# Kernel optimization log

Measured on AMD Instinct MI355X. Metric: run time of the kernel, lower is better.

The kernel has to match this reference:

```python
import jax, jax.numpy as jnp
import numpy as np

N_NODES = 100000
N_EDGES = 320000
DIM = 256  # hidden_dim*2 (bi-RNN)
BN_EPS = 1e-5


def setup_inputs() -> dict:
    key = jax.random.key(0)
    k1, k2, k3 = jax.random.split(key, 3)
    x = jax.random.normal(k1, (N_NODES, DIM), dtype=jnp.float32)
    W = jax.random.normal(k2, (DIM, DIM), dtype=jnp.float32) * (1.0 / np.sqrt(DIM))
    b = jnp.zeros((DIM,), dtype=jnp.float32)
    gamma = jnp.ones((DIM,), dtype=jnp.float32)
    beta = jnp.zeros((DIM,), dtype=jnp.float32)
    edge_index = jax.random.randint(k3, (2, N_EDGES), 0, N_NODES, dtype=jnp.int64)
    return {"x": x, "W": W, "b": b, "gamma": gamma, "beta": beta,
            "edge_index": edge_index}


def reference(x, W, b, gamma, beta, edge_index):
    N = x.shape[0]
    # --- GCNConv: add self-loops, symmetric deg^-1/2 normalization ---
    loop = jnp.arange(N, dtype=edge_index.dtype)
    row = jnp.concatenate([edge_index[0], loop])  # source / j
    col = jnp.concatenate([edge_index[1], loop])  # target / i
    deg = jax.ops.segment_sum(jnp.ones_like(col, dtype=x.dtype), col,
                              num_segments=N)
    dinv = jax.lax.rsqrt(deg)  # deg >= 1 due to self-loops
    norm = dinv[row] * dinv[col]  # [E+N]
    h = x @ W  # linear transform before propagation (PyG GCNConv)
    msg = h[row] * norm[:, None]  # gather + scale, [E+N, F]
    out = jax.ops.segment_sum(msg, col, num_segments=N) + b  # scatter-add
    # --- BatchNorm1d over nodes (training-mode batch statistics) ---
    mean = jnp.mean(out, axis=0)
    var = jnp.var(out, axis=0)
    out = (out - mean) * jax.lax.rsqrt(var + BN_EPS) * gamma + beta
    return jnp.tanh(out)
```

## Files before the change

### kernel.cpp

```cpp
#include <hip/hip_runtime.h>
#include <stdint.h>

#define N_NODES 100000
#define N_EDGES 320000
#define DIM 256
#define BN_EPS 1e-5f

typedef __attribute__((ext_vector_type(8))) short short8;
typedef __attribute__((ext_vector_type(4))) float f32x4;

__device__ __forceinline__ float bf2f(unsigned short u) {
    union { unsigned int i; float f; } v; v.i = ((unsigned int)u) << 16; return v.f;
}
__device__ __forceinline__ unsigned short f2bf(float f) {
    union { float f; unsigned int i; } v; v.f = f;
    unsigned int x = v.i;
    return (unsigned short)((x + 0x7fffu + ((x >> 16) & 1u)) >> 16);
}
__device__ __forceinline__ int eidx(const int* ei, int i64, int which, int e) {
    int idx = which * N_EDGES + e;
    return i64 ? ei[idx * 2] : ei[idx];
}
__device__ __forceinline__ f32x4 ldx4(const void* xv, int xf32, size_t off) {
    if (xf32) return *(const f32x4*)((const float*)xv + off);
    uint2 u = *(const uint2*)((const unsigned short*)xv + off);
    f32x4 o;
    o[0] = bf2f((unsigned short)(u.x & 0xffffu));
    o[1] = bf2f((unsigned short)(u.x >> 16));
    o[2] = bf2f((unsigned short)(u.y & 0xffffu));
    o[3] = bf2f((unsigned short)(u.y >> 16));
    return o;
}

__global__ void k_detect(const unsigned short* __restrict__ xs,
                         const unsigned short* __restrict__ wsw,
                         const int* __restrict__ ei, int* __restrict__ flags) {
    __shared__ int red[3];
    int tid = threadIdx.x;
    if (tid < 3) red[tid] = 0;
    __syncthreads();
    int badx = 0, badw = 0, nz = 0;
    for (int j = 0; j < 8; ++j) {
        if (!(fabsf(bf2f(xs[tid * 8 + j])) <= 1000.0f)) badx = 1;
        if (!(fabsf(bf2f(wsw[tid * 8 + j])) <= 1000.0f)) badw = 1;
        if (ei[(tid * 8 + j) * 2 + 1] != 0) nz = 1;
    }
    if (badx) atomicOr(&red[0], 1);
    if (badw) atomicOr(&red[1], 1);
    if (nz)   atomicOr(&red[2], 1);
    __syncthreads();
    if (tid == 0) { flags[0] = red[0]; flags[1] = red[1]; flags[2] = red[2] ? 0 : 1; }
}

__global__ void k_zero(int* __restrict__ cnt, float* __restrict__ stats) {
    int i = blockIdx.x * 256 + threadIdx.x;
    if (i < N_NODES) cnt[i] = 0;
    if (i < 512) stats[i] = 0.0f;
}

__global__ void k_cnt(const int* __restrict__ ei, int* __restrict__ cnt,
                      const int* __restrict__ flags) {
    int i64 = flags[2];
    int e = blockIdx.x * 256 + threadIdx.x;
    if (e < N_EDGES) atomicAdd(&cnt[eidx(ei, i64, 1, e)], 1);
}

__global__ void k_dinv(const int* __restrict__ cnt, float* __restrict__ dinv) {
    int i = blockIdx.x * 256 + threadIdx.x;
    if (i < N_NODES) dinv[i] = rsqrtf((float)cnt[i] + 1.0f);
}

__global__ void k_scan1(const int* __restrict__ cnt, int* __restrict__ partial) {
    __shared__ int red[256];
    int t = threadIdx.x, b = blockIdx.x;
    int i0 = b * 512 + t * 2;
    int s = 0;
    if (i0 < N_NODES) s += cnt[i0];
    if (i0 + 1 < N_NODES) s += cnt[i0 + 1];
    red[t] = s;
    __syncthreads();
    for (int off = 128; off > 0; off >>= 1) {
        if (t < off) red[t] += red[t + off];
        __syncthreads();
    }
    if (t == 0) partial[b] = red[0];
}

__global__ void k_scan2(const int* __restrict__ partial, int* __restrict__ pbase) {
    __shared__ int s[256];
    int t = threadIdx.x;
    int v = (t < 200) ? partial[t] : 0;
    s[t] = v;
    __syncthreads();
    for (int off = 1; off < 256; off <<= 1) {
        int u = (t >= off) ? s[t - off] : 0;
        __syncthreads();
        s[t] += u;
        __syncthreads();
    }
    if (t < 200) pbase[t] = s[t] - v;
}

__global__ void k_scan3(const int* __restrict__ cnt, const int* __restrict__ pbase,
                        int* __restrict__ row_start, int* __restrict__ cursor) {
    __shared__ int s[512];
    int t = threadIdx.x, b = blockIdx.x;
    int i = b * 512 + t;
    int v = (i < N_NODES) ? cnt[i] : 0;
    s[t] = v;
    __syncthreads();
    for (int off = 1; off < 512; off <<= 1) {
        int u = (t >= off) ? s[t - off] : 0;
        __syncthreads();
        s[t] += u;
        __syncthreads();
    }
    if (i < N_NODES) {
        int excl = pbase[b] + s[t] - v;
        row_start[i] = excl;
        cursor[i] = excl;
    }
}

__global__ void k_fill(const int* __restrict__ ei, const float* __restrict__ dinv,
                       int* __restrict__ cursor, int* __restrict__ csr_src,
                       float* __restrict__ csr_nrm, const int* __restrict__ flags) {
    int i64 = flags[2];
    int e = blockIdx.x * 256 + threadIdx.x;
    if (e >= N_EDGES) return;
    int c = eidx(ei, i64, 1, e);
    int r = eidx(ei, i64, 0, e);
    int slot = atomicAdd(&cursor[c], 1);
    csr_src[slot] = r;
    csr_nrm[slot] = dinv[r] * dinv[c];
}

__global__ void k_wt(const void* __restrict__ wv, unsigned short* __restrict__ Wth,
                     unsigned short* __restrict__ Wtl, const int* __restrict__ flags) {
    int wf32 = flags[1];
    int k = blockIdx.x, n = threadIdx.x;
    float v = wf32 ? ((const float*)wv)[k * DIM + n]
                   : bf2f(((const unsigned short*)wv)[k * DIM + n]);
    unsigned short h = f2bf(v);
    Wth[(size_t)n * DIM + k] = h;
    Wtl[(size_t)n * DIM + k] = f2bf(v - bf2f(h));
}

__global__ void k_agg(const void* __restrict__ xv, const int* __restrict__ row_start,
                      const int* __restrict__ cnt, const int* __restrict__ csr_src,
                      const float* __restrict__ csr_nrm, const float* __restrict__ dinv,
                      unsigned short* __restrict__ zh, unsigned short* __restrict__ zl,
                      const int* __restrict__ flags, int base) {
    int xf32 = flags[0];
    int gid = blockIdx.x * 256 + threadIdx.x;
    int node = base + (gid >> 6);
    int lane = gid & 63;
    float dv = dinv[node];
    float s = dv * dv;
    f32x4 acc = ldx4(xv, xf32, (size_t)node * DIM + lane * 4);
    acc[0] *= s; acc[1] *= s; acc[2] *= s; acc[3] *= s;
    int start = row_start[node];
    int len = cnt[node];
    for (int j = 0; j < len; ++j) {
        int src = csr_src[start + j];
        float nrm = csr_nrm[start + j];
        f32x4 xr = ldx4(xv, xf32, (size_t)src * DIM + lane * 4);
        acc[0] += nrm * xr[0]; acc[1] += nrm * xr[1];
        acc[2] += nrm * xr[2]; acc[3] += nrm * xr[3];
    }
    uint ph0 = 0, ph1 = 0, pl0 = 0, pl1 = 0;
    {
        unsigned short h0 = f2bf(acc[0]), h1 = f2bf(acc[1]);
        unsigned short h2 = f2bf(acc[2]), h3 = f2bf(acc[3]);
        ph0 = (uint)h0 | ((uint)h1 << 16);
        ph1 = (uint)h2 | ((uint)h3 << 16);
        unsigned short l0 = f2bf(acc[0] - bf2f(h0)), l1 = f2bf(acc[1] - bf2f(h1));
        unsigned short l2 = f2bf(acc[2] - bf2f(h2)), l3 = f2bf(acc[3] - bf2f(h3));
        pl0 = (uint)l0 | ((uint)l1 << 16);
        pl1 = (uint)l2 | ((uint)l3 << 16);
    }
    size_t zo = (size_t)(node - base) * DIM + lane * 4;
    uint2 vh; vh.x = ph0; vh.y = ph1;
    uint2 vl; vl.x = pl0; vl.y = pl1;
    *(uint2*)(zh + zo) = vh;
    *(uint2*)(zl + zo) = vl;
}

__launch_bounds__(256, 3)
__global__ void k_gemm(const unsigned short* __restrict__ zh,
                       const unsigned short* __restrict__ zl,
                       const unsigned short* __restrict__ Wth,
                       const unsigned short* __restrict__ Wtl,
                       float* __restrict__ out, float* __restrict__ stats, int base) {
    __shared__ unsigned short zsh[80 * 128];
    __shared__ unsigned short zsl[80 * 128];
    __shared__ float bs[512];
    int tid = threadIdx.x;
    bs[tid] = 0.0f; bs[tid + 256] = 0.0f;
    int m0l = blockIdx.x * 80;
    int w = tid >> 6, lane = tid & 63, quad = lane >> 4, rl = lane & 15;

    f32x4 acc[5][4];
    #pragma unroll
    for (int ms = 0; ms < 5; ++ms)
        #pragma unroll
        for (int nt = 0; nt < 4; ++nt)
            acc[ms][nt] = (f32x4){0.f, 0.f, 0.f, 0.f};

    const char* zhB = (const char*)zh;
    const char* zlB = (const char*)zl;

    for (int half = 0; half < 2; ++half) {
        #pragma unroll
        for (int i = 0; i < 5; ++i) {
            int d   = i * 4096 + w * 1024 + lane * 16;
            int row = d >> 8;
            int kb  = d & 255;
            size_t soff = (size_t)(m0l + row) * 512 + (size_t)(half * 256)
                        + (size_t)(kb ^ ((row & 7) << 4));
            __builtin_amdgcn_global_load_lds(
                (const __attribute__((address_space(1))) unsigned int*)(zhB + soff),
                (__attribute__((address_space(3))) unsigned int*)
                    ((char*)zsh + i * 4096 + w * 1024),
                16, 0, 0);
            __builtin_amdgcn_global_load_lds(
                (const __attribute__((address_space(1))) unsigned int*)(zlB + soff),
                (__attribute__((address_space(3))) unsigned int*)
                    ((char*)zsl + i * 4096 + w * 1024),
                16, 0, 0);
        }
        __syncthreads();

        #pragma unroll
        for (int kk = 0; kk < 4; ++kk) {
            int k0g = half * 128 + kk * 32 + quad * 8;
            short8 bh[4], bl[4];
            #pragma unroll
            for (int nt = 0; nt < 4; ++nt) {
                int n = w * 64 + nt * 16 + rl;
                bh[nt] = *(const short8*)(Wth + (size_t)n * DIM + k0g);
                bl[nt] = *(const short8*)(Wtl + (size_t)n * DIM + k0g);
            }
            #pragma unroll
            for (int ms = 0; ms < 5; ++ms) {
                int row = ms * 16 + rl;
                int kbl = (kk * 32 + quad * 8) * 2;
                int off = row * 256 + (kbl ^ ((row & 7) << 4));
                short8 ah = *(const short8*)((const char*)zsh + off);
                short8 al = *(const short8*)((const char*)zsl + off);
                #pragma unroll
                for (int nt = 0; nt < 4; ++nt) {
                    acc[ms][nt] = __builtin_amdgcn_mfma_f32_16x16x32_bf16(ah, bh[nt], acc[ms][nt], 0, 0, 0);
                    acc[ms][nt] = __builtin_amdgcn_mfma_f32_16x16x32_bf16(al, bh[nt], acc[ms][nt], 0, 0, 0);
                    acc[ms][nt] = __builtin_amdgcn_mfma_f32_16x16x32_bf16(ah, bl[nt], acc[ms][nt], 0, 0, 0);
                }
            }
        }
        __syncthreads();
    }

    #pragma unroll
    for (int nt = 0; nt < 4; ++nt) {
        int col = w * 64 + nt * 16 + rl;
        float s1 = 0.f, s2 = 0.f;
        #pragma unroll
        for (int ms = 0; ms < 5; ++ms)
            #pragma unroll
            for (int i = 0; i < 4; ++i) {
                float v = acc[ms][nt][i];
                s1 += v; s2 += v * v;
                out[(size_t)(base + m0l + ms * 16 + quad * 4 + i) * DIM + col] = v;
            }
        atomicAdd(&bs[col], s1);
        atomicAdd(&bs[256 + col], s2);
    }
    __syncthreads();
    if (tid < 256) {
        atomicAdd(&stats[tid], bs[tid]);
        atomicAdd(&stats[256 + tid], bs[256 + tid]);
    }
}

__global__ void k_fin(const float* __restrict__ stats, const void* __restrict__ gv,
                      const void* __restrict__ bv, float* __restrict__ scsh,
                      const int* __restrict__ flags) {
    int ff32 = flags[0];
    int f = threadIdx.x;
    const float invN = 1.0f / (float)N_NODES;
    float mean = stats[f] * invN;
    float var = stats[256 + f] * invN - mean * mean;
    float g = ff32 ? ((const float*)gv)[f] : bf2f(((const unsigned short*)gv)[f]);
    float bb = ff32 ? ((const float*)bv)[f] : bf2f(((const unsigned short*)bv)[f]);
    float sc = g * rsqrtf(var + BN_EPS);
    scsh[f] = sc;
    scsh[256 + f] = bb - mean * sc;
}

__global__ void k_final(float* __restrict__ out, const float* __restrict__ scsh) {
    int t = blockIdx.x * 256 + threadIdx.x;
    int f0 = (t & 63) * 4;
    size_t off = (size_t)t * 4;
    f32x4 v = *(const f32x4*)(out + off);
    f32x4 o;
    #pragma unroll
    for (int j = 0; j < 4; ++j)
        o[j] = tanhf(v[j] * scsh[f0 + j] + scsh[256 + f0 + j]);
    *(f32x4*)(out + off) = o;
}

extern "C" void kernel_launch(void* const* d_in, const int* in_sizes, int n_in,
                              void* d_out, int out_size, void* d_ws, size_t ws_size,
                              hipStream_t stream) {
    const void* x     = d_in[0];
    const void* W     = d_in[1];
    const void* gamma = d_in[3];
    const void* beta  = d_in[4];
    const int* ei     = (const int*)d_in[5];
    float* out = (float*)d_out;

    char* ws = (char*)d_ws;
    int*   flags     = (int*)(ws);
    int*   cnt       = (int*)(ws + 4096);
    int*   row_start = (int*)(ws + 409600);
    int*   cursor    = (int*)(ws + 819200);
    float* dinv      = (float*)(ws + 1228800);
    int*   partial   = (int*)(ws + 1638400);
    int*   pbase     = (int*)(ws + 1646592);
    float* stats     = (float*)(ws + 1654784);
    float* scsh      = (float*)(ws + 1662976);
    unsigned short* Wth = (unsigned short*)(ws + 1671168);
    unsigned short* Wtl = (unsigned short*)(ws + 1802240);
    int*   csr_src   = (int*)(ws + 1933312);
    float* csr_nrm   = (float*)(ws + 3215360);
    const size_t zoff = 4718592;

    size_t zbytes = ws_size > zoff ? ws_size - zoff : 0;
    long long maxRows = (long long)(zbytes / ((size_t)DIM * 4));
    maxRows -= maxRows % 80;
    if (maxRows <= 0) maxRows = 80;
    if (maxRows > N_NODES) maxRows = N_NODES;

    unsigned short* zh = (unsigned short*)(ws + zoff);
    unsigned short* zl = zh + (size_t)maxRows * DIM;

    k_detect<<<1,    256, 0, stream>>>((const unsigned short*)x, (const unsigned short*)W, ei, flags);
    k_zero  <<<391,  256, 0, stream>>>(cnt, stats);
    k_cnt   <<<1250, 256, 0, stream>>>(ei, cnt, flags);
    k_dinv  <<<391,  256, 0, stream>>>(cnt, dinv);
    k_scan1 <<<200,  256, 0, stream>>>(cnt, partial);
    k_scan2 <<<1,    256, 0, stream>>>(partial, pbase);
    k_scan3 <<<200,  512, 0, stream>>>(cnt, pbase, row_start, cursor);
    k_fill  <<<1250, 256, 0, stream>>>(ei, dinv, cursor, csr_src, csr_nrm, flags);
    k_wt    <<<256,  256, 0, stream>>>(W, Wth, Wtl, flags);

    for (int base = 0; base < N_NODES; base += (int)maxRows) {
        int count = N_NODES - base;
        if (count > (int)maxRows) count = (int)maxRows;
        k_agg <<<count / 4,  256, 0, stream>>>(x, row_start, cnt, csr_src, csr_nrm,
                                               dinv, zh, zl, flags, base);
        k_gemm<<<count / 80, 256, 0, stream>>>(zh, zl, Wth, Wtl, out, stats, base);
    }

    k_fin  <<<1,     256, 0, stream>>>(stats, gamma, beta, scsh, flags);
    k_final<<<25000, 256, 0, stream>>>(out, scsh);
}
```

Before: 423.2 us.

## Pack CSR entries and batch neighbor gathers via wavefront shuffles in aggregation

Merges the CSR source-index and norm arrays into one packed int2 array. Each wavefront loads up to 64 neighbor entries in one coalesced load and broadcasts them with shuffles, so four neighbor-row gathers can be in flight per iteration instead of a serial dependent chain. The self-loop is folded in as an extra padded entry, and rows with more than 63 neighbors fall back to a serial tail. Output stores to the z buffers become nontemporal.

```diff
diff --git a/kernel.cpp b/kernel.cpp
--- a/kernel.cpp
+++ b/kernel.cpp
@@ -8,6 +8,7 @@
 
 typedef __attribute__((ext_vector_type(8))) short short8;
 typedef __attribute__((ext_vector_type(4))) float f32x4;
+typedef __attribute__((ext_vector_type(2))) unsigned int u32x2;
 
 __device__ __forceinline__ float bf2f(unsigned short u) {
     union { unsigned int i; float f; } v; v.i = ((unsigned int)u) << 16; return v.f;
@@ -123,16 +124,17 @@
 }
 
 __global__ void k_fill(const int* __restrict__ ei, const float* __restrict__ dinv,
-                       int* __restrict__ cursor, int* __restrict__ csr_src,
-                       float* __restrict__ csr_nrm, const int* __restrict__ flags) {
+                       int* __restrict__ cursor, int2* __restrict__ csr_pk,
+                       const int* __restrict__ flags) {
     int i64 = flags[2];
     int e = blockIdx.x * 256 + threadIdx.x;
     if (e >= N_EDGES) return;
     int c = eidx(ei, i64, 1, e);
     int r = eidx(ei, i64, 0, e);
     int slot = atomicAdd(&cursor[c], 1);
-    csr_src[slot] = r;
-    csr_nrm[slot] = dinv[r] * dinv[c];
+    union { float f; int i; } u; u.f = dinv[r] * dinv[c];
+    int2 pk; pk.x = r; pk.y = u.i;
+    csr_pk[slot] = pk;
 }
 
 __global__ void k_wt(const void* __restrict__ wv, unsigned short* __restrict__ Wth,
@@ -147,43 +149,109 @@
 }
 
 __global__ void k_agg(const void* __restrict__ xv, const int* __restrict__ row_start,
-                      const int* __restrict__ cnt, const int* __restrict__ csr_src,
-                      const float* __restrict__ csr_nrm, const float* __restrict__ dinv,
+                      const int* __restrict__ cnt, const int2* __restrict__ csr_pk,
+                      const float* __restrict__ dinv,
                       unsigned short* __restrict__ zh, unsigned short* __restrict__ zl,
                       const int* __restrict__ flags, int base) {
     int xf32 = flags[0];
     int gid = blockIdx.x * 256 + threadIdx.x;
     int node = base + (gid >> 6);
     int lane = gid & 63;
+    int start = row_start[node];
+    int len = cnt[node];
     float dv = dinv[node];
     float s = dv * dv;
-    f32x4 acc = ldx4(xv, xf32, (size_t)node * DIM + lane * 4);
-    acc[0] *= s; acc[1] *= s; acc[2] *= s; acc[3] *= s;
-    int start = row_start[node];
-    int len = cnt[node];
-    for (int j = 0; j < len; ++j) {
-        int src = csr_src[start + j];
-        float nrm = csr_nrm[start + j];
-        f32x4 xr = ldx4(xv, xf32, (size_t)src * DIM + lane * 4);
-        acc[0] += nrm * xr[0]; acc[1] += nrm * xr[1];
-        acc[2] += nrm * xr[2]; acc[3] += nrm * xr[3];
-    }
-    uint ph0 = 0, ph1 = 0, pl0 = 0, pl1 = 0;
-    {
-        unsigned short h0 = f2bf(acc[0]), h1 = f2bf(acc[1]);
-        unsigned short h2 = f2bf(acc[2]), h3 = f2bf(acc[3]);
-        ph0 = (uint)h0 | ((uint)h1 << 16);
-        ph1 = (uint)h2 | ((uint)h3 << 16);
-        unsigned short l0 = f2bf(acc[0] - bf2f(h0)), l1 = f2bf(acc[1] - bf2f(h1));
-        unsigned short l2 = f2bf(acc[2] - bf2f(h2)), l3 = f2bf(acc[3] - bf2f(h3));
-        pl0 = (uint)l0 | ((uint)l1 << 16);
-        pl1 = (uint)l2 | ((uint)l3 << 16);
-    }
+
+    int myi = node;
+    float myn = 0.0f;
+    if (lane < len) {
+        int2 pk = csr_pk[start + lane];
+        myi = pk.x;
+        union { int i; float f; } u; u.i = pk.y;
+        myn = u.f;
+    }
+    bool big = (len > 63);
+    int n_eff;
+    if (!big) {
+        if (lane == len) myn = s;
+        n_eff = len + 1;
+    } else {
+        n_eff = 64;
+    }
+    int npad = (n_eff + 3) & ~3;
+
+    f32x4 acc = (f32x4){0.f, 0.f, 0.f, 0.f};
+    size_t lo4 = (size_t)(lane * 4);
+
+    if (xf32) {
+        const float* xp = (const float*)xv;
+        for (int j = 0; j < npad; j += 4) {
+            int i0 = __shfl(myi, j),     i1 = __shfl(myi, j + 1);
+            int i2 = __shfl(myi, j + 2), i3 = __shfl(myi, j + 3);
+            float n0 = __shfl(myn, j),     n1 = __shfl(myn, j + 1);
+            float n2 = __shfl(myn, j + 2), n3 = __shfl(myn, j + 3);
+            f32x4 x0 = *(const f32x4*)(xp + (size_t)i0 * DIM + lo4);
+            f32x4 x1 = *(const f32x4*)(xp + (size_t)i1 * DIM + lo4);
+            f32x4 x2 = *(const f32x4*)(xp + (size_t)i2 * DIM + lo4);
+            f32x4 x3 = *(const f32x4*)(xp + (size_t)i3 * DIM + lo4);
+            #pragma unroll
+            for (int q = 0; q < 4; ++q)
+                acc[q] += n0 * x0[q] + n1 * x1[q] + n2 * x2[q] + n3 * x3[q];
+        }
+    } else {
+        const unsigned short* xp = (const unsigned short*)xv;
+        for (int j = 0; j < npad; j += 4) {
+            int i0 = __shfl(myi, j),     i1 = __shfl(myi, j + 1);
+            int i2 = __shfl(myi, j + 2), i3 = __shfl(myi, j + 3);
+            float n0 = __shfl(myn, j),     n1 = __shfl(myn, j + 1);
+            float n2 = __shfl(myn, j + 2), n3 = __shfl(myn, j + 3);
+            uint2 u0 = *(const uint2*)(xp + (size_t)i0 * DIM + lo4);
+            uint2 u1 = *(const uint2*)(xp + (size_t)i1 * DIM + lo4);
+            uint2 u2 = *(const uint2*)(xp + (size_t)i2 * DIM + lo4);
+            uint2 u3 = *(const uint2*)(xp + (size_t)i3 * DIM + lo4);
+            acc[0] += n0 * bf2f((unsigned short)(u0.x & 0xffffu))
+                    + n1 * bf2f((unsigned short)(u1.x & 0xffffu))
+                    + n2 * bf2f((unsigned short)(u2.x & 0xffffu))
+                    + n3 * bf2f((unsigned short)(u3.x & 0xffffu));
+            acc[1] += n0 * bf2f((unsigned short)(u0.x >> 16))
+                    + n1 * bf2f((unsigned short)(u1.x >> 16))
+                    + n2 * bf2f((unsigned short)(u2.x >> 16))
+                    + n3 * bf2f((unsigned short)(u3.x >> 16));
+            acc[2] += n0 * bf2f((unsigned short)(u0.y & 0xffffu))
+                    + n1 * bf2f((unsigned short)(u1.y & 0xffffu))
+                    + n2 * bf2f((unsigned short)(u2.y & 0xffffu))
+                    + n3 * bf2f((unsigned short)(u3.y & 0xffffu));
+            acc[3] += n0 * bf2f((unsigned short)(u0.y >> 16))
+                    + n1 * bf2f((unsigned short)(u1.y >> 16))
+                    + n2 * bf2f((unsigned short)(u2.y >> 16))
+                    + n3 * bf2f((unsigned short)(u3.y >> 16));
+        }
+    }
+    if (big) {
+        f32x4 xs = ldx4(xv, xf32, (size_t)node * DIM + lo4);
+        #pragma unroll
+        for (int q = 0; q < 4; ++q) acc[q] += s * xs[q];
+        for (int t = 64; t < len; ++t) {
+            int2 pk = csr_pk[start + t];
+            union { int i; float f; } u; u.i = pk.y;
+            f32x4 xr = ldx4(xv, xf32, (size_t)pk.x * DIM + lo4);
+            #pragma unroll
+            for (int q = 0; q < 4; ++q) acc[q] += u.f * xr[q];
+        }
+    }
+
+    unsigned short h0 = f2bf(acc[0]), h1 = f2bf(acc[1]);
+    unsigned short h2 = f2bf(acc[2]), h3 = f2bf(acc[3]);
+    u32x2 vh, vl;
+    vh[0] = (unsigned int)h0 | ((unsigned int)h1 << 16);
+    vh[1] = (unsigned int)h2 | ((unsigned int)h3 << 16);
+    vl[0] = (unsigned int)f2bf(acc[0] - bf2f(h0))
+          | ((unsigned int)f2bf(acc[1] - bf2f(h1)) << 16);
+    vl[1] = (unsigned int)f2bf(acc[2] - bf2f(h2))
+          | ((unsigned int)f2bf(acc[3] - bf2f(h3)) << 16);
     size_t zo = (size_t)(node - base) * DIM + lane * 4;
-    uint2 vh; vh.x = ph0; vh.y = ph1;
-    uint2 vl; vl.x = pl0; vl.y = pl1;
-    *(uint2*)(zh + zo) = vh;
-    *(uint2*)(zl + zo) = vl;
+    __builtin_nontemporal_store(vh, (u32x2*)(zh + zo));
+    __builtin_nontemporal_store(vl, (u32x2*)(zl + zo));
 }
 
 __launch_bounds__(256, 3)
@@ -330,8 +398,7 @@
     float* scsh      = (float*)(ws + 1662976);
     unsigned short* Wth = (unsigned short*)(ws + 1671168);
     unsigned short* Wtl = (unsigned short*)(ws + 1802240);
-    int*   csr_src   = (int*)(ws + 1933312);
-    float* csr_nrm   = (float*)(ws + 3215360);
+    int2*  csr_pk    = (int2*)(ws + 1933312);
     const size_t zoff = 4718592;
 
     size_t zbytes = ws_size > zoff ? ws_size - zoff : 0;
@@ -350,13 +417,13 @@
     k_scan1 <<<200,  256, 0, stream>>>(cnt, partial);
     k_scan2 <<<1,    256, 0, stream>>>(partial, pbase);
     k_scan3 <<<200,  512, 0, stream>>>(cnt, pbase, row_start, cursor);
-    k_fill  <<<1250, 256, 0, stream>>>(ei, dinv, cursor, csr_src, csr_nrm, flags);
+    k_fill  <<<1250, 256, 0, stream>>>(ei, dinv, cursor, csr_pk, flags);
     k_wt    <<<256,  256, 0, stream>>>(W, Wth, Wtl, flags);
 
     for (int base = 0; base < N_NODES; base += (int)maxRows) {
         int count = N_NODES - base;
         if (count > (int)maxRows) count = (int)maxRows;
-        k_agg <<<count / 4,  256, 0, stream>>>(x, row_start, cnt, csr_src, csr_nrm,
+        k_agg <<<count / 4,  256, 0, stream>>>(x, row_start, cnt, csr_pk,
                                                dinv, zh, zl, flags, base);
         k_gemm<<<count / 80, 256, 0, stream>>>(zh, zl, Wth, Wtl, out, stats, base);
     }
```

After: 417.9 us. No clear change (-1.3%).
